# Performance work log

Hardware: AMD Instinct MI355X
Metric: run time of the kernel (lower is better)

Reference implementation:

```python
import jax, jax.numpy as jnp
import numpy as np

DIM = 256
HEADS = 8
HEAD_DIM = 32
INNER = HEADS * HEAD_DIM  # 256
B, L_AG, H, W = 2, 5, 32, 32
SEQ = H * W
POS_HID = 32


def _lin(k, fan_in, fan_out):
    kw, kb = jax.random.split(k)
    Wt = jax.random.normal(kw, (fan_in, fan_out), jnp.float32) * (fan_in ** -0.5)
    b = jax.random.normal(kb, (fan_out,), jnp.float32) * 0.01
    return Wt, b


def setup_inputs() -> dict:
    key = jax.random.key(0)
    ks = jax.random.split(key, 10)
    x = jax.random.normal(ks[0], (B, L_AG, H, W, DIM), jnp.float32)
    Wq, bq = _lin(ks[1], DIM, INNER)
    Wk, bk = _lin(ks[2], DIM, INNER)
    Wv, bv = _lin(ks[3], DIM, INNER)
    Wp1, bp1 = _lin(ks[4], 3, POS_HID)
    Wp2, bp2 = _lin(ks[5], POS_HID, HEADS)
    Ws1, bs1 = _lin(ks[6], DIM, POS_HID)
    Ws2, bs2 = _lin(ks[7], POS_HID, HEADS)
    Wo, bo = _lin(ks[8], INNER, DIM)
    Wg, bg = _lin(ks[9], 2 * DIM, DIM)
    return dict(x=x, Wq=Wq, bq=bq, Wk=Wk, bk=bk, Wv=Wv, bv=bv,
                Wp1=Wp1, bp1=bp1, Wp2=Wp2, bp2=bp2,
                Ws1=Ws1, bs1=bs1, Ws2=Ws2, bs2=bs2,
                Wo=Wo, bo=bo, Wg=Wg, bg=bg)


def _relative_positions(h, w):
    # coords: (h*w, 2), row-major (i//w, i%w) like torch meshgrid 'ij'
    yy, xx = jnp.meshgrid(jnp.arange(h), jnp.arange(w), indexing='ij')
    coords = jnp.stack([yy.reshape(-1), xx.reshape(-1)], axis=-1)  # (L,2)
    rel = (coords[:, None, :] - coords[None, :, :]).astype(jnp.float32)  # (L,L,2)
    dist = jnp.linalg.norm(rel, axis=-1, keepdims=True)  # (L,L,1)
    return jnp.concatenate([rel, dist], axis=-1)  # (L,L,3)


def reference(x, Wq, bq, Wk, bk, Wv, bv, Wp1, bp1, Wp2, bp2,
              Ws1, bs1, Ws2, bs2, Wo, bo, Wg, bg):
    b, l, h, w, c = x.shape
    bl, L = b * l, h * w
    scale = HEAD_DIM ** -0.5
    x2 = x.reshape(bl, L, c)

    q = (x2 @ Wq + bq).reshape(bl, L, HEADS, HEAD_DIM)
    k = (x2 @ Wk + bk).reshape(bl, L, HEADS, HEAD_DIM)
    v = (x2 @ Wv + bv).reshape(bl, L, HEADS, HEAD_DIM)

    scores = jnp.einsum('bihd,bjhd->bhij', q, k) * scale  # (bl,H,L,L)

    rel_pos = _relative_positions(h, w)  # (L,L,3)
    pos_w = jax.nn.relu(rel_pos @ Wp1 + bp1) @ Wp2 + bp2  # (L,L,heads)
    pos_w = jnp.transpose(pos_w, (2, 0, 1))[None]  # (1,heads,L,L)

    s = jax.nn.relu(x2 @ Ws1 + bs1) @ Ws2 + bs2  # (bl,L,heads)
    fsim = jnp.einsum('bih,bjh->bij', s, s)[:, None]  # (bl,1,L,L)

    probs = jax.nn.softmax(scores + pos_w + fsim, axis=-1)
    out = jnp.einsum('bhij,bjhd->bihd', probs, v).reshape(bl, L, INNER)
    out = out @ Wo + bo  # (bl,L,dim); dropout is identity in eval

    gate = jax.nn.sigmoid(jnp.concatenate([x2, out], axis=-1) @ Wg + bg)
    out = gate * out + (1.0 - gate) * x2
    return out.reshape(b, l, h, w, c)
```

## Files before the change

kernel.cpp:

```cpp
#include <hip/hip_runtime.h>

typedef __bf16 bf16_t;
typedef __bf16 bf16x4 __attribute__((ext_vector_type(4)));
typedef __bf16 bf16x8 __attribute__((ext_vector_type(8)));
typedef float  f32x4  __attribute__((ext_vector_type(4)));

#define HEADS 8
#define HEAD_DIM 32
#define DIM 256
#define BL 10
#define SEQ 1024
#define M_TOTAL (BL*SEQ)
#define QK_SCALE 0.17677669529663687f
#define NPOS (63*63)

__device__ __forceinline__ int swz_idx(int row, int col) {
  return row*64 + (col ^ ((row & 7) << 3));
}
__device__ __forceinline__ int swz256(int row, int col) {
  return row*256 + (col ^ ((row & 7) << 3));
}

__global__ __launch_bounds__(256) void cast_kernel(
    const float* __restrict__ x, const float* __restrict__ Ws1,
    const float* __restrict__ bq, const float* __restrict__ bk,
    const float* __restrict__ bv, const float* __restrict__ bs1,
    bf16_t* __restrict__ xb, bf16_t* __restrict__ btall, float* __restrict__ bias_all)
{
  const int NX4 = M_TOTAL*DIM/4;
  const int i = blockIdx.x*blockDim.x + threadIdx.x;
  if (i < NX4) {
    const float4 v = ((const float4*)x)[i];
    bf16x4 o; o[0]=(bf16_t)v.x; o[1]=(bf16_t)v.y; o[2]=(bf16_t)v.z; o[3]=(bf16_t)v.w;
    *(bf16x4*)(xb + (size_t)i*4) = o;
    return;
  }
  int idx = i - NX4;
  if (idx < 8192) {
    const int m = idx >> 8, k = idx & 255;
    btall[(768 + m)*256 + k] = (bf16_t)Ws1[k*32 + m];
    return;
  }
  idx -= 8192;
  if (idx < 832) {
    bias_all[idx] = (idx < 256) ? bq[idx] : (idx < 512) ? bk[idx-256] :
                    (idx < 768) ? bv[idx-512] : (idx < 800) ? bs1[idx-768] : 0.f;
  }
}

__global__ __launch_bounds__(256) void trans_kernel(
    const float* __restrict__ Wq, const float* __restrict__ Wk, const float* __restrict__ Wv,
    const float* __restrict__ Wo, const float* __restrict__ Wg,
    bf16_t* __restrict__ btall, bf16_t* __restrict__ wot,
    bf16_t* __restrict__ wg1t, bf16_t* __restrict__ wg2t)
{
  __shared__ float tile[64][65];
  const float* src; bf16_t* dst;
  switch (blockIdx.z) {
    case 0: src = Wq;         dst = btall;          break;
    case 1: src = Wk;         dst = btall + 65536;  break;
    case 2: src = Wv;         dst = btall + 131072; break;
    case 3: src = Wo;         dst = wot;            break;
    case 4: src = Wg;         dst = wg1t;           break;
    default: src = Wg + 65536; dst = wg2t;          break;
  }
  const int bi = blockIdx.x, bj = blockIdx.y;
  const int t = threadIdx.x, tr = t >> 4, tc = t & 15;
  #pragma unroll
  for (int i = 0; i < 4; ++i) {
    const float4 v = *(const float4*)(src + (size_t)(bi*64 + tr + 16*i)*256 + bj*64 + tc*4);
    float* tp = &tile[tr + 16*i][tc*4];
    tp[0]=v.x; tp[1]=v.y; tp[2]=v.z; tp[3]=v.w;
  }
  __syncthreads();
  #pragma unroll
  for (int i = 0; i < 4; ++i) {
    bf16x4 o;
    #pragma unroll
    for (int e = 0; e < 4; ++e) o[e] = (bf16_t)tile[tc*4 + e][tr + 16*i];
    *(bf16x4*)(dst + (size_t)(bj*64 + tr + 16*i)*256 + bi*64 + tc*4) = o;
  }
}

__global__ __launch_bounds__(256) void pos_tab_kernel(
    const float* __restrict__ Wp1, const float* __restrict__ bp1,
    const float* __restrict__ Wp2, const float* __restrict__ bp2,
    float* __restrict__ posT)
{
  __shared__ float w1[96], b1[32], w2[256], b2[8];
  const int tid = threadIdx.x;
  if (tid < 96) w1[tid] = Wp1[tid];
  if (tid < 32) b1[tid] = bp1[tid];
  w2[tid] = Wp2[tid];
  if (tid < 8)  b2[tid] = bp2[tid];
  __syncthreads();
  const int p = blockIdx.x*256 + tid;
  if (p >= NPOS) return;
  const float dy = (float)(p / 63 - 31);
  const float dx = (float)(p % 63 - 31);
  const float dist = sqrtf(dy*dy + dx*dx);
  float o[8];
  #pragma unroll
  for (int t = 0; t < 8; ++t) o[t] = b2[t];
  #pragma unroll
  for (int m = 0; m < 32; ++m) {
    float hv = fmaf(dy, w1[m], fmaf(dx, w1[32+m], fmaf(dist, w1[64+m], b1[m])));
    hv = fmaxf(hv, 0.f);
    #pragma unroll
    for (int t = 0; t < 8; ++t) o[t] = fmaf(hv, w2[m*8+t], o[t]);
  }
  #pragma unroll
  for (int t = 0; t < 8; ++t) posT[t*NPOS + p] = o[t];
}

__global__ __launch_bounds__(256) void qkv_kernel(
    const bf16_t* __restrict__ xb, const bf16_t* __restrict__ btall,
    const float* __restrict__ bias_all,
    bf16_t* __restrict__ qbuf, bf16_t* __restrict__ kbuf, bf16_t* __restrict__ vbuf,
    float* __restrict__ hidf)
{
  const int mt = blockIdx.x, ngb = blockIdx.y;
  const int tid = threadIdx.x;
  const int w = tid >> 6, lane = tid & 63, g = lane >> 4, l15 = lane & 15;
  const int arow = mt*64 + w*16 + l15;
  const bf16x8* Arow = (const bf16x8*)(xb + (size_t)arow*DIM);
  bf16x8 af[8];
  #pragma unroll
  for (int kc = 0; kc < 8; ++kc) af[kc] = Arow[kc*4 + g];
  const bool ishid = (ngb == 12);
  const int cmax = ishid ? 2 : 4;
  bf16_t* dst = (ngb < 4) ? qbuf : (ngb < 8) ? kbuf : vbuf;
  const int coloff = (ngb & 3) * 64;
  const float scale = (ngb < 4) ? QK_SCALE : 1.f;
  for (int c = 0; c < cmax; ++c) {
    const int n = ngb*64 + c*16 + l15;
    const bf16x8* Brow = (const bf16x8*)(btall + (size_t)n*DIM);
    f32x4 acc = {0.f,0.f,0.f,0.f};
    #pragma unroll
    for (int kc = 0; kc < 8; ++kc)
      acc = __builtin_amdgcn_mfma_f32_16x16x32_bf16(af[kc], Brow[kc*4+g], acc, 0, 0, 0);
    const float bvv = bias_all[n];
    #pragma unroll
    for (int r = 0; r < 4; ++r) {
      const int row = mt*64 + w*16 + g*4 + r;
      const float val = acc[r] + bvv;
      if (ishid) hidf[(size_t)row*32 + c*16 + l15] = fmaxf(val, 0.f);
      else dst[(size_t)row*DIM + coloff + c*16 + l15] = (bf16_t)(val*scale);
    }
  }
}

__global__ __launch_bounds__(256) void s2_kernel(
    const float* __restrict__ hidf, const float* __restrict__ Ws2,
    const float* __restrict__ bs2, float* __restrict__ sf)
{
  const int row = blockIdx.x*blockDim.x + threadIdx.x;
  if (row >= M_TOTAL) return;
  const float4* h4 = (const float4*)(hidf + (size_t)row*32);
  float sv[8];
  #pragma unroll
  for (int t = 0; t < 8; ++t) sv[t] = bs2[t];
  #pragma unroll
  for (int mq = 0; mq < 8; ++mq) {
    const float4 h = h4[mq];
    const float hv[4] = {h.x, h.y, h.z, h.w};
    #pragma unroll
    for (int e = 0; e < 4; ++e) {
      #pragma unroll
      for (int t = 0; t < 8; ++t) sv[t] = fmaf(hv[e], Ws2[(mq*4+e)*8+t], sv[t]);
    }
  }
  #pragma unroll
  for (int t = 0; t < 8; ++t) sf[(size_t)row*8+t] = sv[t];
}

__global__ __launch_bounds__(256) void attn_kernel(
    const bf16_t* __restrict__ qb, const bf16_t* __restrict__ kb,
    const bf16_t* __restrict__ vb, const float* __restrict__ sf,
    const float* __restrict__ posT, bf16_t* __restrict__ att)
{
  __shared__ __align__(16) bf16_t lqp[64*64];
  __shared__ __align__(16) bf16_t lk[64*64];
  __shared__ __align__(16) bf16_t lv[48*64];
  __shared__ float ptab[33*63];

  const int wg = blockIdx.x;
  const int xcd = wg & 7, within = wg >> 3;
  const int pair = xcd*10 + (within >> 4);
  const int it = within & 15;
  const int h = pair & 7, b = pair >> 3;
  const int i0 = it*64, iy0 = it*2;
  const int tid = threadIdx.x;
  const int w = tid >> 6, lane = tid & 63, g = lane >> 4, l15 = lane & 15;
  const int r4 = tid >> 2, q4 = tid & 3;

  bf16x8 kreg = *(const bf16x8*)(kb + (size_t)(b*SEQ + r4)*DIM + h*HEAD_DIM + q4*8);
  bf16x8 vreg = *(const bf16x8*)(vb + (size_t)(b*SEQ + r4)*DIM + h*HEAD_DIM + q4*8);
  float4 sA, sB;
  if (tid < 64) {
    const float* sp = sf + (size_t)(b*SEQ + tid)*8;
    sA = *(const float4*)sp; sB = *(const float4*)(sp + 4);
  }

  for (int p = tid; p < 33*63; p += 256) {
    const int rr = p / 63, cc = p - rr*63;
    ptab[p] = posT[h*NPOS + (iy0 + rr)*63 + cc];
  }
  for (int p = tid; p < 16*64; p += 256) {
    const int d = 32 + (p >> 6), j = p & 63;
    lv[d*64 + (j ^ ((d & 7) << 3))] = (bf16_t)((d == 32) ? 1.f : 0.f);
  }
  for (int p = tid; p < 192; p += 256) {
    const int rr = p / 3, ch = 5 + (p % 3);
    bf16x8 z;
    #pragma unroll
    for (int e = 0; e < 8; ++e) z[e] = (bf16_t)0.f;
    *(bf16x8*)&lk[swz_idx(rr, ch*8)] = z;
  }
  {
    const int grow = b*SEQ + i0 + r4;
    #pragma unroll
    for (int cc = 0; cc < 2; ++cc) {
      const int ch = q4*2 + cc;
      bf16x8 v;
      if (ch < 4) {
        v = *(const bf16x8*)(qb + (size_t)grow*DIM + h*HEAD_DIM + ch*8);
      } else if (ch == 4) {
        const float* sp = sf + (size_t)grow*8;
        #pragma unroll
        for (int e = 0; e < 8; ++e) v[e] = (bf16_t)sp[e];
      } else {
        #pragma unroll
        for (int e = 0; e < 8; ++e) v[e] = (bf16_t)0.f;
      }
      *(bf16x8*)&lqp[swz_idx(r4, ch*8)] = v;
    }
  }
  __syncthreads();

  const int qrow = w*16 + l15;
  const bf16x8 aq0 = *(const bf16x8*)&lqp[swz_idx(qrow, g*8)];
  const bf16x8 aq1 = *(const bf16x8*)&lqp[swz_idx(qrow, 32 + g*8)];

  f32x4 accO0 = {0.f,0.f,0.f,0.f}, accO1 = {0.f,0.f,0.f,0.f}, accO2 = {0.f,0.f,0.f,0.f};
  float mrow[4];
  #pragma unroll
  for (int r = 0; r < 4; ++r) mrow[r] = -1e30f;

  for (int jt = 0; jt < 16; ++jt) {
    const int j0 = jt*64;
    __syncthreads();
    *(bf16x8*)&lk[swz_idx(r4, q4*8)] = kreg;
    #pragma unroll
    for (int e = 0; e < 8; ++e) {
      const int d = q4*8 + e;
      lv[d*64 + (r4 ^ ((d & 7) << 3))] = vreg[e];
    }
    if (tid < 64) {
      bf16x8 sv;
      sv[0]=(bf16_t)sA.x; sv[1]=(bf16_t)sA.y; sv[2]=(bf16_t)sA.z; sv[3]=(bf16_t)sA.w;
      sv[4]=(bf16_t)sB.x; sv[5]=(bf16_t)sB.y; sv[6]=(bf16_t)sB.z; sv[7]=(bf16_t)sB.w;
      *(bf16x8*)&lk[swz_idx(tid, 32)] = sv;
    }
    __syncthreads();

    if (jt < 15) {
      const int grow = b*SEQ + j0 + 64 + r4;
      kreg = *(const bf16x8*)(kb + (size_t)grow*DIM + h*HEAD_DIM + q4*8);
      vreg = *(const bf16x8*)(vb + (size_t)grow*DIM + h*HEAD_DIM + q4*8);
      if (tid < 64) {
        const float* sp = sf + (size_t)(b*SEQ + j0 + 64 + tid)*8;
        sA = *(const float4*)sp; sB = *(const float4*)(sp + 4);
      }
    }

    f32x4 s4[4];
    #pragma unroll
    for (int c = 0; c < 4; ++c) {
      const int krow = c*16 + l15;
      const bf16x8 bk0 = *(const bf16x8*)&lk[swz_idx(krow, g*8)];
      const bf16x8 bk1 = *(const bf16x8*)&lk[swz_idx(krow, 32 + g*8)];
      f32x4 acc = {0.f,0.f,0.f,0.f};
      acc = __builtin_amdgcn_mfma_f32_16x16x32_bf16(aq0, bk0, acc, 0, 0, 0);
      acc = __builtin_amdgcn_mfma_f32_16x16x32_bf16(aq1, bk1, acc, 0, 0, 0);
      s4[c] = acc;
    }

    const int ib = i0 + w*16 + g*4;
    #pragma unroll
    for (int r = 0; r < 4; ++r) {
      const int rbase = ((ib + r) >> 5) - iy0 + 31;
      const int ixr = (ib + r) & 31;
      #pragma unroll
      for (int c = 0; c < 4; ++c) {
        const int j = j0 + c*16 + l15;
        s4[c][r] += ptab[(rbase - (j >> 5))*63 + (ixr - (j & 31) + 31)];
      }
    }

    float pmax[4];
    #pragma unroll
    for (int r = 0; r < 4; ++r)
      pmax[r] = fmaxf(fmaxf(s4[0][r], s4[1][r]), fmaxf(s4[2][r], s4[3][r]));
    #pragma unroll
    for (int mk = 1; mk <= 8; mk <<= 1) {
      #pragma unroll
      for (int r = 0; r < 4; ++r)
        pmax[r] = fmaxf(pmax[r], __shfl_xor(pmax[r], mk));
    }
    float alpha[4];
    #pragma unroll
    for (int r = 0; r < 4; ++r) {
      const float mn = fmaxf(mrow[r], pmax[r]);
      alpha[r] = __expf(mrow[r] - mn);
      mrow[r] = mn;
    }
    #pragma unroll
    for (int r = 0; r < 4; ++r) {
      #pragma unroll
      for (int c = 0; c < 4; ++c) s4[c][r] = __expf(s4[c][r] - mrow[r]);
      accO0[r] *= alpha[r];
      accO1[r] *= alpha[r];
      accO2[r] *= alpha[r];
    }

    #pragma unroll
    for (int c = 0; c < 4; ++c) {
      #pragma unroll
      for (int r = 0; r < 4; ++r)
        lqp[swz_idx(w*16 + g*4 + r, c*16 + l15)] = (bf16_t)s4[c][r];
    }

    const int prow = w*16 + l15;
    #pragma unroll
    for (int kc = 0; kc < 2; ++kc) {
      const bf16x8 ap  = *(const bf16x8*)&lqp[swz_idx(prow, kc*32 + g*8)];
      const bf16x8 bv0 = *(const bf16x8*)&lv[swz_idx(l15,      kc*32 + g*8)];
      const bf16x8 bv1 = *(const bf16x8*)&lv[swz_idx(16 + l15, kc*32 + g*8)];
      const bf16x8 bv2 = *(const bf16x8*)&lv[swz_idx(32 + l15, kc*32 + g*8)];
      accO0 = __builtin_amdgcn_mfma_f32_16x16x32_bf16(ap, bv0, accO0, 0, 0, 0);
      accO1 = __builtin_amdgcn_mfma_f32_16x16x32_bf16(ap, bv1, accO1, 0, 0, 0);
      accO2 = __builtin_amdgcn_mfma_f32_16x16x32_bf16(ap, bv2, accO2, 0, 0, 0);
    }
  }

  #pragma unroll
  for (int r = 0; r < 4; ++r) {
    const int row = b*SEQ + i0 + w*16 + g*4 + r;
    const float lsum = __shfl(accO2[r], lane & 48);
    const float inv = 1.f / lsum;
    att[(size_t)row*DIM + h*HEAD_DIM + l15]      = (bf16_t)(accO0[r]*inv);
    att[(size_t)row*DIM + h*HEAD_DIM + 16 + l15] = (bf16_t)(accO1[r]*inv);
  }
}

__global__ __launch_bounds__(256) void prjgate_kernel(
    const bf16_t* __restrict__ att, const bf16_t* __restrict__ wot,
    const float* __restrict__ bo, const bf16_t* __restrict__ xb,
    const float* __restrict__ x, const bf16_t* __restrict__ wg1t,
    const bf16_t* __restrict__ wg2t, const float* __restrict__ bg,
    float* __restrict__ outp)
{
  __shared__ __align__(16) bf16_t prjT[16*256];
  const int row0 = blockIdx.x * 16;
  const int tid = threadIdx.x;
  const int w = tid >> 6, lane = tid & 63, g = lane >> 4, l15 = lane & 15;
  const int arow = row0 + l15;

  {
    const bf16x8* Arow = (const bf16x8*)(att + (size_t)arow*DIM);
    bf16x8 afA[8];
    #pragma unroll
    for (int kc = 0; kc < 8; ++kc) afA[kc] = Arow[kc*4 + g];
    #pragma unroll
    for (int ct = 0; ct < 4; ++ct) {
      const int n = w*64 + ct*16 + l15;
      const bf16x8* Brow = (const bf16x8*)(wot + (size_t)n*DIM);
      f32x4 acc = {0.f,0.f,0.f,0.f};
      #pragma unroll
      for (int kc = 0; kc < 8; ++kc)
        acc = __builtin_amdgcn_mfma_f32_16x16x32_bf16(afA[kc], Brow[kc*4+g], acc, 0, 0, 0);
      const float bvo = bo[n];
      #pragma unroll
      for (int r = 0; r < 4; ++r)
        prjT[swz256(g*4 + r, n)] = (bf16_t)(acc[r] + bvo);
    }
  }
  __syncthreads();

  const bf16x8* A1r = (const bf16x8*)(xb + (size_t)arow*DIM);
  bf16x8 a1[8], a2[8];
  #pragma unroll
  for (int kc = 0; kc < 8; ++kc) {
    a1[kc] = A1r[kc*4 + g];
    a2[kc] = *(const bf16x8*)&prjT[swz256(l15, kc*32 + g*8)];
  }
  #pragma unroll
  for (int ct = 0; ct < 4; ++ct) {
    const int n = w*64 + ct*16 + l15;
    const bf16x8* b1 = (const bf16x8*)(wg1t + (size_t)n*DIM);
    const bf16x8* b2 = (const bf16x8*)(wg2t + (size_t)n*DIM);
    f32x4 acc = {0.f,0.f,0.f,0.f};
    #pragma unroll
    for (int kc = 0; kc < 8; ++kc)
      acc = __builtin_amdgcn_mfma_f32_16x16x32_bf16(a1[kc], b1[kc*4+g], acc, 0, 0, 0);
    #pragma unroll
    for (int kc = 0; kc < 8; ++kc)
      acc = __builtin_amdgcn_mfma_f32_16x16x32_bf16(a2[kc], b2[kc*4+g], acc, 0, 0, 0);
    const float bgv = bg[n];
    #pragma unroll
    for (int r = 0; r < 4; ++r) {
      const int grow = row0 + g*4 + r;
      const float gate = 1.f / (1.f + __expf(-(acc[r] + bgv)));
      const float pv = (float)prjT[swz256(g*4 + r, n)];
      const float xv = x[(size_t)grow*DIM + n];
      outp[(size_t)grow*DIM + n] = gate*pv + (1.f - gate)*xv;
    }
  }
}

extern "C" void kernel_launch(void* const* d_in, const int* in_sizes, int n_in,
                              void* d_out, int out_size, void* d_ws, size_t ws_size,
                              hipStream_t stream)
{
  const float* x   = (const float*)d_in[0];
  const float* Wq  = (const float*)d_in[1];
  const float* bq  = (const float*)d_in[2];
  const float* Wk  = (const float*)d_in[3];
  const float* bk  = (const float*)d_in[4];
  const float* Wv  = (const float*)d_in[5];
  const float* bv  = (const float*)d_in[6];
  const float* Wp1 = (const float*)d_in[7];
  const float* bp1 = (const float*)d_in[8];
  const float* Wp2 = (const float*)d_in[9];
  const float* bp2 = (const float*)d_in[10];
  const float* Ws1 = (const float*)d_in[11];
  const float* bs1 = (const float*)d_in[12];
  const float* Ws2 = (const float*)d_in[13];
  const float* bs2 = (const float*)d_in[14];
  const float* Wo  = (const float*)d_in[15];
  const float* bo  = (const float*)d_in[16];
  const float* Wg  = (const float*)d_in[17];
  const float* bg  = (const float*)d_in[18];

  char* ws = (char*)d_ws;
  size_t off = 0;
  auto alloc = [&](size_t bytes) {
    char* p = ws + off;
    off += (bytes + 255) & ~(size_t)255;
    return p;
  };
  bf16_t* xb    = (bf16_t*)alloc((size_t)M_TOTAL*DIM*2);
  bf16_t* qbuf  = (bf16_t*)alloc((size_t)M_TOTAL*DIM*2);
  bf16_t* kbuf  = (bf16_t*)alloc((size_t)M_TOTAL*DIM*2);
  bf16_t* vbuf  = (bf16_t*)alloc((size_t)M_TOTAL*DIM*2);
  bf16_t* att   = (bf16_t*)alloc((size_t)M_TOTAL*DIM*2);
  bf16_t* btall = (bf16_t*)alloc((size_t)800*256*2);
  bf16_t* wot   = (bf16_t*)alloc(65536*2);
  bf16_t* wg1t  = (bf16_t*)alloc(65536*2);
  bf16_t* wg2t  = (bf16_t*)alloc(65536*2);
  float*  bias_all = (float*)alloc(832*4);
  float*  hidf  = (float*)alloc((size_t)M_TOTAL*32*4);
  float*  sfb   = (float*)alloc((size_t)M_TOTAL*8*4);
  float*  posT  = (float*)alloc((size_t)HEADS*NPOS*4);
  (void)ws_size; (void)in_sizes; (void)n_in; (void)out_size;

  const int cast_total = M_TOTAL*DIM/4 + 8192 + 832;
  cast_kernel<<<(cast_total + 255)/256, 256, 0, stream>>>(x, Ws1, bq, bk, bv, bs1,
                                                          xb, btall, bias_all);
  trans_kernel<<<dim3(4,4,6), 256, 0, stream>>>(Wq, Wk, Wv, Wo, Wg,
                                                btall, wot, wg1t, wg2t);
  pos_tab_kernel<<<(NPOS+255)/256, 256, 0, stream>>>(Wp1, bp1, Wp2, bp2, posT);
  qkv_kernel<<<dim3(M_TOTAL/64, 13), 256, 0, stream>>>(xb, btall, bias_all,
                                                       qbuf, kbuf, vbuf, hidf);
  s2_kernel<<<M_TOTAL/256, 256, 0, stream>>>(hidf, Ws2, bs2, sfb);
  attn_kernel<<<SEQ/64*HEADS*BL, 256, 0, stream>>>(qbuf, kbuf, vbuf, sfb, posT, att);
  prjgate_kernel<<<M_TOTAL/16, 256, 0, stream>>>(att, wot, bo, xb, x, wg1t, wg2t, bg,
                                                 (float*)d_out);
}
```

Before: 167.2 us.

## Merge prep kernels, use exp2 softmax with lazy rescale, prefetch pos bias to registers

Merges the cast, transpose and positional-table kernels into one launch to cut launch overhead. Folds log2(e) into the Q scale, the s features and the pos table so the softmax can use exp2f. Rescaling of the running max is skipped unless the new max exceeds the old one by more than 8, and the relative-position bias is now read from global memory into registers one tile ahead instead of being staged in an LDS table. The lazy rescale lets exponent values grow up to 2^8 before rescaling, and the global gathers replace LDS reads.

```diff
diff --git a/kernel.cpp b/kernel.cpp
--- a/kernel.cpp
+++ b/kernel.cpp
@@ -12,7 +12,13 @@
 #define SEQ 1024
 #define M_TOTAL (BL*SEQ)
 #define QK_SCALE 0.17677669529663687f
+#define LOG2E 1.4426950408889634f
+#define SQRT_LOG2E 1.2011224087864498f
 #define NPOS (63*63)
+
+#define NCAST 2596
+#define NTRANS 96
+#define NPREP (NCAST + NTRANS + 16)
 
 __device__ __forceinline__ int swz_idx(int row, int col) {
   return row*64 + (col ^ ((row & 7) << 3));
@@ -21,96 +27,101 @@
   return row*256 + (col ^ ((row & 7) << 3));
 }
 
-__global__ __launch_bounds__(256) void cast_kernel(
+__global__ __launch_bounds__(256) void prep_all_kernel(
     const float* __restrict__ x, const float* __restrict__ Ws1,
     const float* __restrict__ bq, const float* __restrict__ bk,
     const float* __restrict__ bv, const float* __restrict__ bs1,
-    bf16_t* __restrict__ xb, bf16_t* __restrict__ btall, float* __restrict__ bias_all)
-{
-  const int NX4 = M_TOTAL*DIM/4;
-  const int i = blockIdx.x*blockDim.x + threadIdx.x;
-  if (i < NX4) {
-    const float4 v = ((const float4*)x)[i];
-    bf16x4 o; o[0]=(bf16_t)v.x; o[1]=(bf16_t)v.y; o[2]=(bf16_t)v.z; o[3]=(bf16_t)v.w;
-    *(bf16x4*)(xb + (size_t)i*4) = o;
-    return;
-  }
-  int idx = i - NX4;
-  if (idx < 8192) {
-    const int m = idx >> 8, k = idx & 255;
-    btall[(768 + m)*256 + k] = (bf16_t)Ws1[k*32 + m];
-    return;
-  }
-  idx -= 8192;
-  if (idx < 832) {
-    bias_all[idx] = (idx < 256) ? bq[idx] : (idx < 512) ? bk[idx-256] :
-                    (idx < 768) ? bv[idx-512] : (idx < 800) ? bs1[idx-768] : 0.f;
-  }
-}
-
-__global__ __launch_bounds__(256) void trans_kernel(
     const float* __restrict__ Wq, const float* __restrict__ Wk, const float* __restrict__ Wv,
     const float* __restrict__ Wo, const float* __restrict__ Wg,
-    bf16_t* __restrict__ btall, bf16_t* __restrict__ wot,
-    bf16_t* __restrict__ wg1t, bf16_t* __restrict__ wg2t)
+    const float* __restrict__ Wp1, const float* __restrict__ bp1,
+    const float* __restrict__ Wp2, const float* __restrict__ bp2,
+    bf16_t* __restrict__ xb, bf16_t* __restrict__ btall, float* __restrict__ bias_all,
+    bf16_t* __restrict__ wot, bf16_t* __restrict__ wg1t, bf16_t* __restrict__ wg2t,
+    float* __restrict__ posT)
 {
   __shared__ float tile[64][65];
-  const float* src; bf16_t* dst;
-  switch (blockIdx.z) {
-    case 0: src = Wq;         dst = btall;          break;
-    case 1: src = Wk;         dst = btall + 65536;  break;
-    case 2: src = Wv;         dst = btall + 131072; break;
-    case 3: src = Wo;         dst = wot;            break;
-    case 4: src = Wg;         dst = wg1t;           break;
-    default: src = Wg + 65536; dst = wg2t;          break;
-  }
-  const int bi = blockIdx.x, bj = blockIdx.y;
-  const int t = threadIdx.x, tr = t >> 4, tc = t & 15;
-  #pragma unroll
-  for (int i = 0; i < 4; ++i) {
-    const float4 v = *(const float4*)(src + (size_t)(bi*64 + tr + 16*i)*256 + bj*64 + tc*4);
-    float* tp = &tile[tr + 16*i][tc*4];
-    tp[0]=v.x; tp[1]=v.y; tp[2]=v.z; tp[3]=v.w;
-  }
-  __syncthreads();
-  #pragma unroll
-  for (int i = 0; i < 4; ++i) {
-    bf16x4 o;
-    #pragma unroll
-    for (int e = 0; e < 4; ++e) o[e] = (bf16_t)tile[tc*4 + e][tr + 16*i];
-    *(bf16x4*)(dst + (size_t)(bj*64 + tr + 16*i)*256 + bi*64 + tc*4) = o;
-  }
-}
-
-__global__ __launch_bounds__(256) void pos_tab_kernel(
-    const float* __restrict__ Wp1, const float* __restrict__ bp1,
-    const float* __restrict__ Wp2, const float* __restrict__ bp2,
-    float* __restrict__ posT)
-{
-  __shared__ float w1[96], b1[32], w2[256], b2[8];
+  const int bid = blockIdx.x;
   const int tid = threadIdx.x;
-  if (tid < 96) w1[tid] = Wp1[tid];
-  if (tid < 32) b1[tid] = bp1[tid];
-  w2[tid] = Wp2[tid];
-  if (tid < 8)  b2[tid] = bp2[tid];
-  __syncthreads();
-  const int p = blockIdx.x*256 + tid;
-  if (p >= NPOS) return;
-  const float dy = (float)(p / 63 - 31);
-  const float dx = (float)(p % 63 - 31);
-  const float dist = sqrtf(dy*dy + dx*dx);
-  float o[8];
-  #pragma unroll
-  for (int t = 0; t < 8; ++t) o[t] = b2[t];
-  #pragma unroll
-  for (int m = 0; m < 32; ++m) {
-    float hv = fmaf(dy, w1[m], fmaf(dx, w1[32+m], fmaf(dist, w1[64+m], b1[m])));
-    hv = fmaxf(hv, 0.f);
-    #pragma unroll
-    for (int t = 0; t < 8; ++t) o[t] = fmaf(hv, w2[m*8+t], o[t]);
-  }
-  #pragma unroll
-  for (int t = 0; t < 8; ++t) posT[t*NPOS + p] = o[t];
+
+  if (bid < NCAST) {
+    const int NX4 = M_TOTAL*DIM/4;
+    const int i = bid*256 + tid;
+    if (i < NX4) {
+      const float4 v = ((const float4*)x)[i];
+      bf16x4 o; o[0]=(bf16_t)v.x; o[1]=(bf16_t)v.y; o[2]=(bf16_t)v.z; o[3]=(bf16_t)v.w;
+      *(bf16x4*)(xb + (size_t)i*4) = o;
+      return;
+    }
+    int idx = i - NX4;
+    if (idx < 8192) {
+      const int m = idx >> 8, k = idx & 255;
+      btall[(768 + m)*256 + k] = (bf16_t)Ws1[k*32 + m];
+      return;
+    }
+    idx -= 8192;
+    if (idx < 832) {
+      bias_all[idx] = (idx < 256) ? bq[idx] : (idx < 512) ? bk[idx-256] :
+                      (idx < 768) ? bv[idx-512] : (idx < 800) ? bs1[idx-768] : 0.f;
+    }
+    return;
+  }
+
+  if (bid < NCAST + NTRANS) {
+    const int t0 = bid - NCAST;
+    const int z = t0 >> 4, bi = (t0 & 15) >> 2, bj = t0 & 3;
+    const float* src; bf16_t* dst;
+    switch (z) {
+      case 0: src = Wq;          dst = btall;          break;
+      case 1: src = Wk;          dst = btall + 65536;  break;
+      case 2: src = Wv;          dst = btall + 131072; break;
+      case 3: src = Wo;          dst = wot;            break;
+      case 4: src = Wg;          dst = wg1t;           break;
+      default: src = Wg + 65536; dst = wg2t;           break;
+    }
+    const int tr = tid >> 4, tc = tid & 15;
+    #pragma unroll
+    for (int i = 0; i < 4; ++i) {
+      const float4 v = *(const float4*)(src + (size_t)(bi*64 + tr + 16*i)*256 + bj*64 + tc*4);
+      float* tp = &tile[tr + 16*i][tc*4];
+      tp[0]=v.x; tp[1]=v.y; tp[2]=v.z; tp[3]=v.w;
+    }
+    __syncthreads();
+    #pragma unroll
+    for (int i = 0; i < 4; ++i) {
+      bf16x4 o;
+      #pragma unroll
+      for (int e = 0; e < 4; ++e) o[e] = (bf16_t)tile[tc*4 + e][tr + 16*i];
+      *(bf16x4*)(dst + (size_t)(bj*64 + tr + 16*i)*256 + bi*64 + tc*4) = o;
+    }
+    return;
+  }
+
+  {
+    float* sm = &tile[0][0];
+    float* w1 = sm; float* b1 = sm + 96; float* w2 = sm + 128; float* b2 = sm + 384;
+    if (tid < 96) w1[tid] = Wp1[tid];
+    if (tid < 32) b1[tid] = bp1[tid];
+    w2[tid] = Wp2[tid];
+    if (tid < 8)  b2[tid] = bp2[tid];
+    __syncthreads();
+    const int p = (bid - NCAST - NTRANS)*256 + tid;
+    if (p >= NPOS) return;
+    const float dy = (float)(p / 63 - 31);
+    const float dx = (float)(p % 63 - 31);
+    const float dist = sqrtf(dy*dy + dx*dx);
+    float o[8];
+    #pragma unroll
+    for (int t = 0; t < 8; ++t) o[t] = b2[t];
+    #pragma unroll
+    for (int m = 0; m < 32; ++m) {
+      float hv = fmaf(dy, w1[m], fmaf(dx, w1[32+m], fmaf(dist, w1[64+m], b1[m])));
+      hv = fmaxf(hv, 0.f);
+      #pragma unroll
+      for (int t = 0; t < 8; ++t) o[t] = fmaf(hv, w2[m*8+t], o[t]);
+    }
+    #pragma unroll
+    for (int t = 0; t < 8; ++t) posT[t*NPOS + p] = o[t]*LOG2E;
+  }
 }
 
 __global__ __launch_bounds__(256) void qkv_kernel(
@@ -131,7 +142,7 @@
   const int cmax = ishid ? 2 : 4;
   bf16_t* dst = (ngb < 4) ? qbuf : (ngb < 8) ? kbuf : vbuf;
   const int coloff = (ngb & 3) * 64;
-  const float scale = (ngb < 4) ? QK_SCALE : 1.f;
+  const float scale = (ngb < 4) ? QK_SCALE*LOG2E : 1.f;
   for (int c = 0; c < cmax; ++c) {
     const int n = ngb*64 + c*16 + l15;
     const bf16x8* Brow = (const bf16x8*)(btall + (size_t)n*DIM);
@@ -171,7 +182,7 @@
     }
   }
   #pragma unroll
-  for (int t = 0; t < 8; ++t) sf[(size_t)row*8+t] = sv[t];
+  for (int t = 0; t < 8; ++t) sf[(size_t)row*8+t] = sv[t]*SQRT_LOG2E;
 }
 
 __global__ __launch_bounds__(256) void attn_kernel(
@@ -182,17 +193,24 @@
   __shared__ __align__(16) bf16_t lqp[64*64];
   __shared__ __align__(16) bf16_t lk[64*64];
   __shared__ __align__(16) bf16_t lv[48*64];
-  __shared__ float ptab[33*63];
 
   const int wg = blockIdx.x;
   const int xcd = wg & 7, within = wg >> 3;
   const int pair = xcd*10 + (within >> 4);
   const int it = within & 15;
   const int h = pair & 7, b = pair >> 3;
-  const int i0 = it*64, iy0 = it*2;
+  const int i0 = it*64;
   const int tid = threadIdx.x;
   const int w = tid >> 6, lane = tid & 63, g = lane >> 4, l15 = lane & 15;
   const int r4 = tid >> 2, q4 = tid & 3;
+
+  const float* posTh = posT + h*NPOS;
+  int Cr[4];
+  #pragma unroll
+  for (int r = 0; r < 4; ++r) {
+    const int irow = i0 + w*16 + g*4 + r;
+    Cr[r] = ((irow >> 5) + 31)*63 + (irow & 31) + 31;
+  }
 
   bf16x8 kreg = *(const bf16x8*)(kb + (size_t)(b*SEQ + r4)*DIM + h*HEAD_DIM + q4*8);
   bf16x8 vreg = *(const bf16x8*)(vb + (size_t)(b*SEQ + r4)*DIM + h*HEAD_DIM + q4*8);
@@ -201,11 +219,15 @@
     const float* sp = sf + (size_t)(b*SEQ + tid)*8;
     sA = *(const float4*)sp; sB = *(const float4*)(sp + 4);
   }
-
-  for (int p = tid; p < 33*63; p += 256) {
-    const int rr = p / 63, cc = p - rr*63;
-    ptab[p] = posT[h*NPOS + (iy0 + rr)*63 + cc];
-  }
+  float pf[4][4];
+  #pragma unroll
+  for (int c = 0; c < 4; ++c) {
+    const int j = c*16 + l15;
+    const int gj = (j >> 5)*63 + (j & 31);
+    #pragma unroll
+    for (int r = 0; r < 4; ++r) pf[c][r] = posTh[Cr[r] - gj];
+  }
+
   for (int p = tid; p < 16*64; p += 256) {
     const int d = 32 + (p >> 6), j = p & 63;
     lv[d*64 + (j ^ ((d & 7) << 3))] = (bf16_t)((d == 32) ? 1.f : 0.f);
@@ -286,15 +308,18 @@
       s4[c] = acc;
     }
 
-    const int ib = i0 + w*16 + g*4;
-    #pragma unroll
-    for (int r = 0; r < 4; ++r) {
-      const int rbase = ((ib + r) >> 5) - iy0 + 31;
-      const int ixr = (ib + r) & 31;
+    #pragma unroll
+    for (int c = 0; c < 4; ++c) {
+      #pragma unroll
+      for (int r = 0; r < 4; ++r) s4[c][r] += pf[c][r];
+    }
+    if (jt < 15) {
       #pragma unroll
       for (int c = 0; c < 4; ++c) {
-        const int j = j0 + c*16 + l15;
-        s4[c][r] += ptab[(rbase - (j >> 5))*63 + (ixr - (j & 31) + 31)];
+        const int j = j0 + 64 + c*16 + l15;
+        const int gj = (j >> 5)*63 + (j & 31);
+        #pragma unroll
+        for (int r = 0; r < 4; ++r) pf[c][r] = posTh[Cr[r] - gj];
       }
     }
 
@@ -308,20 +333,22 @@
       for (int r = 0; r < 4; ++r)
         pmax[r] = fmaxf(pmax[r], __shfl_xor(pmax[r], mk));
     }
-    float alpha[4];
+    bool need = false;
+    #pragma unroll
+    for (int r = 0; r < 4; ++r) need = need || (pmax[r] > mrow[r] + 8.f);
+    if (__any(need)) {
+      #pragma unroll
+      for (int r = 0; r < 4; ++r) {
+        const float mn = fmaxf(mrow[r], pmax[r]);
+        const float alpha = exp2f(mrow[r] - mn);
+        mrow[r] = mn;
+        accO0[r] *= alpha; accO1[r] *= alpha; accO2[r] *= alpha;
+      }
+    }
     #pragma unroll
     for (int r = 0; r < 4; ++r) {
-      const float mn = fmaxf(mrow[r], pmax[r]);
-      alpha[r] = __expf(mrow[r] - mn);
-      mrow[r] = mn;
-    }
-    #pragma unroll
-    for (int r = 0; r < 4; ++r) {
-      #pragma unroll
-      for (int c = 0; c < 4; ++c) s4[c][r] = __expf(s4[c][r] - mrow[r]);
-      accO0[r] *= alpha[r];
-      accO1[r] *= alpha[r];
-      accO2[r] *= alpha[r];
+      #pragma unroll
+      for (int c = 0; c < 4; ++c) s4[c][r] = exp2f(s4[c][r] - mrow[r]);
     }
 
     #pragma unroll
@@ -465,12 +492,9 @@
   float*  posT  = (float*)alloc((size_t)HEADS*NPOS*4);
   (void)ws_size; (void)in_sizes; (void)n_in; (void)out_size;
 
-  const int cast_total = M_TOTAL*DIM/4 + 8192 + 832;
-  cast_kernel<<<(cast_total + 255)/256, 256, 0, stream>>>(x, Ws1, bq, bk, bv, bs1,
-                                                          xb, btall, bias_all);
-  trans_kernel<<<dim3(4,4,6), 256, 0, stream>>>(Wq, Wk, Wv, Wo, Wg,
-                                                btall, wot, wg1t, wg2t);
-  pos_tab_kernel<<<(NPOS+255)/256, 256, 0, stream>>>(Wp1, bp1, Wp2, bp2, posT);
+  prep_all_kernel<<<NPREP, 256, 0, stream>>>(x, Ws1, bq, bk, bv, bs1,
+                                             Wq, Wk, Wv, Wo, Wg, Wp1, bp1, Wp2, bp2,
+                                             xb, btall, bias_all, wot, wg1t, wg2t, posT);
   qkv_kernel<<<dim3(M_TOTAL/64, 13), 256, 0, stream>>>(xb, btall, bias_all,
                                                        qbuf, kbuf, vbuf, hidf);
   s2_kernel<<<M_TOTAL/256, 256, 0, stream>>>(hidf, Ws2, bs2, sfb);
```

Result: no change. 170.1 us (+1.7%).
